# Kernel tuning notes

Hardware: AMD Instinct MI355X
Metric: run time of the kernel (lower is better)

The kernel has to match this reference:

```python
import jax, jax.numpy as jnp
import numpy as np

D_MODEL = 1024
NUM_HEADS = 16
DILATION = 2
SEG = 2048


def setup_inputs() -> dict:
    key = jax.random.key(0)
    k1, k2, k3, k4, k5 = jax.random.split(key, 5)
    B, S, D = 2, 8192, D_MODEL
    scale = 1.0 / np.sqrt(D)
    x = jax.random.normal(k1, (B, S, D), dtype=jnp.float32)
    wqkv = jax.random.normal(k2, (D, 3 * D), dtype=jnp.float32) * scale
    bqkv = jnp.zeros((3 * D,), dtype=jnp.float32)
    wo = jax.random.normal(k3, (D, D), dtype=jnp.float32) * scale
    bo = jnp.zeros((D,), dtype=jnp.float32)
    return {"x": x, "wqkv": wqkv, "bqkv": bqkv, "wo": wo, "bo": bo}


def reference(x, wqkv, bqkv, wo, bo):
    B, S, D = x.shape
    H = NUM_HEADS
    hd = D // H
    # segment reshape + dilated strided slice: [B, N, L, D]
    xs = x.reshape(B, -1, SEG, D)[:, :, ::DILATION, :]
    Bn, N, L, _ = xs.shape
    # fused QKV projection
    qkv = xs @ wqkv + bqkv                       # [B, N, L, 3D]
    q, k, v = jnp.split(qkv, 3, axis=-1)
    q = q.reshape(B, N, L, H, hd)
    k = k.reshape(B, N, L, H, hd)
    v = v.reshape(B, N, L, H, hd)
    scale = 1.0 / jnp.sqrt(jnp.asarray(hd, dtype=x.dtype))
    scores = jnp.einsum("bnqhd,bnkhd->bnhqk", q, k) * scale
    attn = jax.nn.softmax(scores, axis=-1)
    out = jnp.einsum("bnhqk,bnkhd->bnqhd", attn, v).reshape(B, N, L, D)
    out = out @ wo + bo                          # out projection
    return out.reshape(B, N * L, D)
```

## Files before the change

kernel.cpp:

```cpp
#include <hip/hip_runtime.h>
#include <hip/hip_bf16.h>
#include <stdint.h>

typedef __attribute__((ext_vector_type(8))) short short8;
typedef __attribute__((ext_vector_type(4))) float float4v;
typedef __attribute__((ext_vector_type(4))) unsigned int uint4v;
typedef unsigned short u16;

#if __has_builtin(__builtin_amdgcn_exp2f)
#define EXP2F(x) __builtin_amdgcn_exp2f(x)
#else
#define EXP2F(x) __expf(0.69314718056f * (x))
#endif

__device__ __forceinline__ u16 f2b(float f) {
    union { __hip_bfloat16 b; u16 u; } cv;
    cv.b = __float2bfloat16(f);
    return cv.u;
}

#define GLD16(g, l) __builtin_amdgcn_global_load_lds( \
    (const __attribute__((address_space(1))) void*)(g), \
    (__attribute__((address_space(3))) void*)(l), 16, 0, 0)

__global__ void convert_x(const float* __restrict__ x, u16* __restrict__ xb) {
    int id = blockIdx.x * 256 + threadIdx.x;
    int row = id >> 8;
    int c4 = id & 255;
    const float4* src = reinterpret_cast<const float4*>(x + (size_t)(2 * row) * 1024) + c4;
    float4 v = *src;
    ushort4 o;
    o.x = f2b(v.x); o.y = f2b(v.y); o.z = f2b(v.z); o.w = f2b(v.w);
    *(reinterpret_cast<ushort4*>(xb + (size_t)row * 1024) + c4) = o;
}

__global__ void transpose_convert(const float* __restrict__ in, u16* __restrict__ out,
                                  int K, int N) {
    __shared__ float tile[32][33];
    int n0 = blockIdx.x * 32, k0 = blockIdx.y * 32;
    int tx = threadIdx.x, ty = threadIdx.y;
#pragma unroll
    for (int i = 0; i < 4; i++)
        tile[ty + i * 8][tx] = in[(size_t)(k0 + ty + i * 8) * N + n0 + tx];
    __syncthreads();
#pragma unroll
    for (int i = 0; i < 4; i++)
        out[(size_t)(n0 + ty + i * 8) * K + k0 + tx] = f2b(tile[tx][ty + i * 8]);
}

template <int MODE>
__global__ __launch_bounds__(256) void gemm_bt(
    const u16* __restrict__ A, const u16* __restrict__ BT,
    const float* __restrict__ bias,
    float* __restrict__ Cf, u16* __restrict__ Cqk, u16* __restrict__ Cvt,
    int M, int N, int K) {
    __shared__ u16 As[128 * 32];
    __shared__ u16 Bs[128 * 32];
    const int tid = threadIdx.x;
    const int w = tid >> 6, l = tid & 63;
    const int q = l >> 4, c = l & 15;
    const int m0 = blockIdx.y * 128, n0 = blockIdx.x * 128;
    const int wm = (w >> 1) * 64, wn = (w & 1) * 64;

    const int srow = w * 16 + (l >> 2);
    const int scol = (l & 3) * 8;
    const u16* gA = A + (size_t)(m0 + srow) * K + scol;
    const u16* gB = BT + (size_t)(n0 + srow) * K + scol;

    float4v acc[4][4];
#pragma unroll
    for (int i = 0; i < 4; i++)
#pragma unroll
        for (int j = 0; j < 4; j++) acc[i][j] = {0.f, 0.f, 0.f, 0.f};

    char* AsB = (char*)&As[0];
    char* BsB = (char*)&Bs[0];

    for (int k0 = 0; k0 < K; k0 += 32) {
        __syncthreads();
        GLD16(gA + k0,                  AsB + w * 1024);
        GLD16(gA + (size_t)64 * K + k0, AsB + 4096 + w * 1024);
        GLD16(gB + k0,                  BsB + w * 1024);
        GLD16(gB + (size_t)64 * K + k0, BsB + 4096 + w * 1024);
        __syncthreads();
        short8 af[4], bf[4];
#pragma unroll
        for (int mt = 0; mt < 4; mt++)
            af[mt] = *reinterpret_cast<const short8*>(&As[(wm + mt * 16 + c) * 32 + q * 8]);
#pragma unroll
        for (int nt = 0; nt < 4; nt++)
            bf[nt] = *reinterpret_cast<const short8*>(&Bs[(wn + nt * 16 + c) * 32 + q * 8]);
#pragma unroll
        for (int mt = 0; mt < 4; mt++)
#pragma unroll
            for (int nt = 0; nt < 4; nt++)
                acc[mt][nt] = __builtin_amdgcn_mfma_f32_16x16x32_bf16(af[mt], bf[nt], acc[mt][nt], 0, 0, 0);
    }

    const int q4 = q * 4;
    if (MODE == 0) {
#pragma unroll
        for (int nt = 0; nt < 4; nt++) {
            int col = n0 + wn + nt * 16 + c;
            float bv = bias[col];
#pragma unroll
            for (int mt = 0; mt < 4; mt++) {
                int row = m0 + wm + mt * 16 + q4;
#pragma unroll
                for (int r = 0; r < 4; r++)
                    Cf[(size_t)(row + r) * N + col] = acc[mt][nt][r] + bv;
            }
        }
    } else {
        bool isV = (n0 + wn) >= 2048;
        float qscale = ((n0 + wn) < 1024) ? (0.125f * 1.44269504f) : 1.0f;
#pragma unroll
        for (int nt = 0; nt < 4; nt++) {
            int col = n0 + wn + nt * 16 + c;
            float bv = bias[col];
            if (!isV) {
#pragma unroll
                for (int mt = 0; mt < 4; mt++) {
                    int row = m0 + wm + mt * 16 + q4;
#pragma unroll
                    for (int r = 0; r < 4; r++)
                        Cqk[(size_t)(row + r) * 2048 + col] = f2b((acc[mt][nt][r] + bv) * qscale);
                }
            } else {
                int hd_ = col - 2048;
#pragma unroll
                for (int mt = 0; mt < 4; mt++) {
                    int row = m0 + wm + mt * 16 + q4;
                    int bn = row >> 10, key = row & 1023;
                    ushort4 pk;
                    pk.x = f2b(acc[mt][nt][0] + bv);
                    pk.y = f2b(acc[mt][nt][1] + bv);
                    pk.z = f2b(acc[mt][nt][2] + bv);
                    pk.w = f2b(acc[mt][nt][3] + bv);
                    *reinterpret_cast<ushort4*>(
                        &Cvt[((size_t)(bn << 10) + hd_) * 1024 + key]) = pk;
                }
            }
        }
    }
}

__global__ __launch_bounds__(256) void attn(const u16* __restrict__ qk,
                                            const u16* __restrict__ vt,
                                            u16* __restrict__ ob) {
    __shared__ u16 Ks[64 * 72];
    __shared__ u16 Vs[80 * 72];
    __shared__ u16 Ps[128 * 72];
    const int tid = threadIdx.x;
    const int w = tid >> 6, l = tid & 63, q = l >> 4, c = l & 15;
    const int qtile = blockIdx.x, combo = blockIdx.y;
    const int bn = combo >> 4, h = combo & 15;
    const int t0 = bn << 10;
    const int qoff = h << 6;
    const int koff = 1024 + (h << 6);
    const int vrow0 = combo << 6;
    const int qrow_base = t0 + qtile * 128 + w * 32;

    for (int idx = tid; idx < 16 * 72; idx += 256) {
        int rr = idx / 72, cc = idx - rr * 72;
        Vs[(64 + rr) * 72 + cc] = (rr == 0) ? (u16)0x3F80 : (u16)0;
    }

    short8 aq[2][2];
#pragma unroll
    for (int mt = 0; mt < 2; mt++)
#pragma unroll
        for (int ks = 0; ks < 2; ks++)
            aq[mt][ks] = *reinterpret_cast<const short8*>(
                qk + (size_t)(qrow_base + mt * 16 + c) * 2048 + qoff + ks * 32 + q * 8);

    float4v o_acc[2][4];
    float4v osum[2];
#pragma unroll
    for (int mt = 0; mt < 2; mt++) {
#pragma unroll
        for (int nt = 0; nt < 4; nt++) o_acc[mt][nt] = {0.f, 0.f, 0.f, 0.f};
        osum[mt] = {0.f, 0.f, 0.f, 0.f};
    }

    const int sr = tid >> 3;
    const int sc = (tid & 7) * 8;

    for (int chunk = 0; chunk < 16; chunk++) {
        const int key0 = chunk * 64;
        __syncthreads();
#pragma unroll
        for (int i = 0; i < 2; i++) {
            int r = sr + i * 32;
            uint4v kv = *reinterpret_cast<const uint4v*>(
                qk + (size_t)(t0 + key0 + r) * 2048 + koff + sc);
            *reinterpret_cast<uint4v*>(&Ks[r * 72 + sc]) = kv;
            uint4v vv = *reinterpret_cast<const uint4v*>(
                vt + (size_t)(vrow0 + r) * 1024 + key0 + sc);
            *reinterpret_cast<uint4v*>(&Vs[r * 72 + sc]) = vv;
        }
        __syncthreads();

        float4v s[2][4];
#pragma unroll
        for (int mt = 0; mt < 2; mt++)
#pragma unroll
            for (int nt = 0; nt < 4; nt++) s[mt][nt] = {0.f, 0.f, 0.f, 0.f};
#pragma unroll
        for (int ks = 0; ks < 2; ks++) {
            short8 bk[4];
#pragma unroll
            for (int nt = 0; nt < 4; nt++)
                bk[nt] = *reinterpret_cast<const short8*>(&Ks[(nt * 16 + c) * 72 + ks * 32 + q * 8]);
#pragma unroll
            for (int mt = 0; mt < 2; mt++)
#pragma unroll
                for (int nt = 0; nt < 4; nt++)
                    s[mt][nt] = __builtin_amdgcn_mfma_f32_16x16x32_bf16(aq[mt][ks], bk[nt], s[mt][nt], 0, 0, 0);
        }

#pragma unroll
        for (int mt = 0; mt < 2; mt++)
#pragma unroll
            for (int r = 0; r < 4; r++)
#pragma unroll
                for (int nt = 0; nt < 4; nt++)
                    Ps[(w * 32 + mt * 16 + q * 4 + r) * 72 + nt * 16 + c] =
                        f2b(EXP2F(s[mt][nt][r]));

#pragma unroll
        for (int ks = 0; ks < 2; ks++) {
            short8 pf[2], vf[4], v1;
#pragma unroll
            for (int mt = 0; mt < 2; mt++)
                pf[mt] = *reinterpret_cast<const short8*>(&Ps[(w * 32 + mt * 16 + c) * 72 + ks * 32 + q * 8]);
#pragma unroll
            for (int nt = 0; nt < 4; nt++)
                vf[nt] = *reinterpret_cast<const short8*>(&Vs[(nt * 16 + c) * 72 + ks * 32 + q * 8]);
            v1 = *reinterpret_cast<const short8*>(&Vs[(64 + c) * 72 + ks * 32 + q * 8]);
#pragma unroll
            for (int mt = 0; mt < 2; mt++) {
#pragma unroll
                for (int nt = 0; nt < 4; nt++)
                    o_acc[mt][nt] = __builtin_amdgcn_mfma_f32_16x16x32_bf16(pf[mt], vf[nt], o_acc[mt][nt], 0, 0, 0);
                osum[mt] = __builtin_amdgcn_mfma_f32_16x16x32_bf16(pf[mt], v1, osum[mt], 0, 0, 0);
            }
        }
    }

#pragma unroll
    for (int mt = 0; mt < 2; mt++) {
        float inv[4];
#pragma unroll
        for (int r = 0; r < 4; r++) {
            float lv = __shfl(osum[mt][r], tid & 48);
            inv[r] = 1.0f / lv;
        }
#pragma unroll
        for (int nt = 0; nt < 4; nt++)
#pragma unroll
            for (int r = 0; r < 4; r++) {
                int row = qrow_base + mt * 16 + q * 4 + r;
                int col = (h << 6) + nt * 16 + c;
                ob[(size_t)row * 1024 + col] = f2b(o_acc[mt][nt][r] * inv[r]);
            }
    }
}

extern "C" void kernel_launch(void* const* d_in, const int* in_sizes, int n_in,
                              void* d_out, int out_size, void* d_ws, size_t ws_size,
                              hipStream_t stream) {
    const float* x    = (const float*)d_in[0];
    const float* wqkv = (const float*)d_in[1];
    const float* bqkv = (const float*)d_in[2];
    const float* wo   = (const float*)d_in[3];
    const float* bo   = (const float*)d_in[4];
    float* out = (float*)d_out;
    char* ws = (char*)d_ws;

    u16* xb    = (u16*)(ws);
    u16* wqkvT = (u16*)(ws + 16777216);
    u16* woT   = (u16*)(ws + 23068672);
    u16* qkb   = (u16*)(ws + 25165824);
    u16* vtb   = (u16*)(ws + 58720256);
    u16* obuf  = (u16*)(ws + 75497472);

    convert_x<<<8192, 256, 0, stream>>>(x, xb);
    transpose_convert<<<dim3(96, 32), dim3(32, 8), 0, stream>>>(wqkv, wqkvT, 1024, 3072);
    transpose_convert<<<dim3(32, 32), dim3(32, 8), 0, stream>>>(wo, woT, 1024, 1024);
    gemm_bt<1><<<dim3(24, 64), 256, 0, stream>>>(xb, wqkvT, bqkv,
                                                 nullptr, qkb, vtb, 8192, 3072, 1024);
    attn<<<dim3(8, 128), 256, 0, stream>>>(qkb, vtb, obuf);
    gemm_bt<0><<<dim3(8, 64), 256, 0, stream>>>(obuf, woT, bo,
                                                out, nullptr, nullptr, 8192, 1024, 1024);
}
```

Baseline: 306.4 us.

## Load K/V MFMA fragments directly from global, dropping LDS staging and barriers

The attention kernel no longer stages each 64-key K and V chunk in shared memory. Each wave now loads its MFMA B-operand fragments straight from global memory into registers, which removes both per-chunk __syncthreads and the shared-memory round trip. The row-sum 'ones' operand is now built in registers rather than read from a padded LDS row. The cost is that all four waves fetch the same K/V data separately, so L1/L2 traffic rises and the reads are less coalesced. Global load latency is also now exposed directly in the inner loop.

```diff
diff --git a/kernel.cpp b/kernel.cpp
--- a/kernel.cpp
+++ b/kernel.cpp
@@ -148,8 +148,6 @@
 __global__ __launch_bounds__(256) void attn(const u16* __restrict__ qk,
                                             const u16* __restrict__ vt,
                                             u16* __restrict__ ob) {
-    __shared__ u16 Ks[64 * 72];
-    __shared__ u16 Vs[80 * 72];
     __shared__ u16 Ps[128 * 72];
     const int tid = threadIdx.x;
     const int w = tid >> 6, l = tid & 63, q = l >> 4, c = l & 15;
@@ -161,9 +159,11 @@
     const int vrow0 = combo << 6;
     const int qrow_base = t0 + qtile * 128 + w * 32;
 
-    for (int idx = tid; idx < 16 * 72; idx += 256) {
-        int rr = idx / 72, cc = idx - rr * 72;
-        Vs[(64 + rr) * 72 + cc] = (rr == 0) ? (u16)0x3F80 : (u16)0;
+    short8 v1;
+    {
+        u16 one = (c == 0) ? (u16)0x3F80 : (u16)0;
+#pragma unroll
+        for (int j = 0; j < 8; j++) v1[j] = (short)one;
     }
 
     short8 aq[2][2];
@@ -183,23 +183,19 @@
         osum[mt] = {0.f, 0.f, 0.f, 0.f};
     }
 
-    const int sr = tid >> 3;
-    const int sc = (tid & 7) * 8;
+    const u16* kfrag = qk + (size_t)(t0 + c) * 2048 + koff + q * 8;
+    const u16* vfrag = vt + (size_t)(vrow0 + c) * 1024 + q * 8;
 
     for (int chunk = 0; chunk < 16; chunk++) {
         const int key0 = chunk * 64;
-        __syncthreads();
-#pragma unroll
-        for (int i = 0; i < 2; i++) {
-            int r = sr + i * 32;
-            uint4v kv = *reinterpret_cast<const uint4v*>(
-                qk + (size_t)(t0 + key0 + r) * 2048 + koff + sc);
-            *reinterpret_cast<uint4v*>(&Ks[r * 72 + sc]) = kv;
-            uint4v vv = *reinterpret_cast<const uint4v*>(
-                vt + (size_t)(vrow0 + r) * 1024 + key0 + sc);
-            *reinterpret_cast<uint4v*>(&Vs[r * 72 + sc]) = vv;
-        }
-        __syncthreads();
+
+        short8 bk[2][4];
+#pragma unroll
+        for (int ks = 0; ks < 2; ks++)
+#pragma unroll
+            for (int nt = 0; nt < 4; nt++)
+                bk[ks][nt] = *reinterpret_cast<const short8*>(
+                    kfrag + (size_t)(key0 + nt * 16) * 2048 + ks * 32);
 
         float4v s[2][4];
 #pragma unroll
@@ -207,17 +203,20 @@
 #pragma unroll
             for (int nt = 0; nt < 4; nt++) s[mt][nt] = {0.f, 0.f, 0.f, 0.f};
 #pragma unroll
-        for (int ks = 0; ks < 2; ks++) {
-            short8 bk[4];
+        for (int ks = 0; ks < 2; ks++)
+#pragma unroll
+            for (int mt = 0; mt < 2; mt++)
+#pragma unroll
+                for (int nt = 0; nt < 4; nt++)
+                    s[mt][nt] = __builtin_amdgcn_mfma_f32_16x16x32_bf16(aq[mt][ks], bk[ks][nt], s[mt][nt], 0, 0, 0);
+
+        short8 vf[2][4];
+#pragma unroll
+        for (int ks = 0; ks < 2; ks++)
 #pragma unroll
             for (int nt = 0; nt < 4; nt++)
-                bk[nt] = *reinterpret_cast<const short8*>(&Ks[(nt * 16 + c) * 72 + ks * 32 + q * 8]);
-#pragma unroll
-            for (int mt = 0; mt < 2; mt++)
-#pragma unroll
-                for (int nt = 0; nt < 4; nt++)
-                    s[mt][nt] = __builtin_amdgcn_mfma_f32_16x16x32_bf16(aq[mt][ks], bk[nt], s[mt][nt], 0, 0, 0);
-        }
+                vf[ks][nt] = *reinterpret_cast<const short8*>(
+                    vfrag + (size_t)(nt * 16) * 1024 + key0 + ks * 32);
 
 #pragma unroll
         for (int mt = 0; mt < 2; mt++)
@@ -230,19 +229,16 @@
 
 #pragma unroll
         for (int ks = 0; ks < 2; ks++) {
-            short8 pf[2], vf[4], v1;
+            short8 pf[2];
 #pragma unroll
             for (int mt = 0; mt < 2; mt++)
-                pf[mt] = *reinterpret_cast<const short8*>(&Ps[(w * 32 + mt * 16 + c) * 72 + ks * 32 + q * 8]);
-#pragma unroll
-            for (int nt = 0; nt < 4; nt++)
-                vf[nt] = *reinterpret_cast<const short8*>(&Vs[(nt * 16 + c) * 72 + ks * 32 + q * 8]);
-            v1 = *reinterpret_cast<const short8*>(&Vs[(64 + c) * 72 + ks * 32 + q * 8]);
+                pf[mt] = *reinterpret_cast<const short8*>(
+                    &Ps[(w * 32 + mt * 16 + c) * 72 + ks * 32 + q * 8]);
 #pragma unroll
             for (int mt = 0; mt < 2; mt++) {
 #pragma unroll
                 for (int nt = 0; nt < 4; nt++)
-                    o_acc[mt][nt] = __builtin_amdgcn_mfma_f32_16x16x32_bf16(pf[mt], vf[nt], o_acc[mt][nt], 0, 0, 0);
+                    o_acc[mt][nt] = __builtin_amdgcn_mfma_f32_16x16x32_bf16(pf[mt], vf[ks][nt], o_acc[mt][nt], 0, 0, 0);
                 osum[mt] = __builtin_amdgcn_mfma_f32_16x16x32_bf16(pf[mt], v1, osum[mt], 0, 0, 0);
             }
         }
```

Measured after the change: 366.0 us. +19.5%, slower.

## Prefetch next K/V chunk into registers and build ones-vector in registers

Applied to the files above, without the earlier changes.

The attention kernel now issues the global loads for the next 64-key K/V chunk into registers before computing the current chunk. It writes them to shared memory after the PV MFMAs, so global latency overlaps with compute. The constant ones-vector used for the row-sum MFMA is built directly in registers instead of being stored in and read from an extra LDS region. This raises register pressure and keeps two barriers per iteration.

```diff
diff --git a/kernel.cpp b/kernel.cpp
--- a/kernel.cpp
+++ b/kernel.cpp
@@ -149,7 +149,7 @@
                                             const u16* __restrict__ vt,
                                             u16* __restrict__ ob) {
     __shared__ u16 Ks[64 * 72];
-    __shared__ u16 Vs[80 * 72];
+    __shared__ u16 Vs[64 * 72];
     __shared__ u16 Ps[128 * 72];
     const int tid = threadIdx.x;
     const int w = tid >> 6, l = tid & 63, q = l >> 4, c = l & 15;
@@ -161,9 +161,11 @@
     const int vrow0 = combo << 6;
     const int qrow_base = t0 + qtile * 128 + w * 32;
 
-    for (int idx = tid; idx < 16 * 72; idx += 256) {
-        int rr = idx / 72, cc = idx - rr * 72;
-        Vs[(64 + rr) * 72 + cc] = (rr == 0) ? (u16)0x3F80 : (u16)0;
+    short8 v1;
+    {
+        u16 one = (c == 0) ? (u16)0x3F80 : (u16)0;
+#pragma unroll
+        for (int j = 0; j < 8; j++) v1[j] = (short)one;
     }
 
     short8 aq[2][2];
@@ -186,20 +188,35 @@
     const int sr = tid >> 3;
     const int sc = (tid & 7) * 8;
 
+    uint4v kreg[2], vreg[2];
+#pragma unroll
+    for (int i = 0; i < 2; i++) {
+        int r = sr + i * 32;
+        kreg[i] = *reinterpret_cast<const uint4v*>(
+            qk + (size_t)(t0 + r) * 2048 + koff + sc);
+        vreg[i] = *reinterpret_cast<const uint4v*>(
+            vt + (size_t)(vrow0 + r) * 1024 + sc);
+    }
+#pragma unroll
+    for (int i = 0; i < 2; i++) {
+        int r = sr + i * 32;
+        *reinterpret_cast<uint4v*>(&Ks[r * 72 + sc]) = kreg[i];
+        *reinterpret_cast<uint4v*>(&Vs[r * 72 + sc]) = vreg[i];
+    }
+    __syncthreads();
+
     for (int chunk = 0; chunk < 16; chunk++) {
-        const int key0 = chunk * 64;
-        __syncthreads();
-#pragma unroll
-        for (int i = 0; i < 2; i++) {
-            int r = sr + i * 32;
-            uint4v kv = *reinterpret_cast<const uint4v*>(
-                qk + (size_t)(t0 + key0 + r) * 2048 + koff + sc);
-            *reinterpret_cast<uint4v*>(&Ks[r * 72 + sc]) = kv;
-            uint4v vv = *reinterpret_cast<const uint4v*>(
-                vt + (size_t)(vrow0 + r) * 1024 + key0 + sc);
-            *reinterpret_cast<uint4v*>(&Vs[r * 72 + sc]) = vv;
-        }
-        __syncthreads();
+        if (chunk < 15) {
+            const int key0n = (chunk + 1) * 64;
+#pragma unroll
+            for (int i = 0; i < 2; i++) {
+                int r = sr + i * 32;
+                kreg[i] = *reinterpret_cast<const uint4v*>(
+                    qk + (size_t)(t0 + key0n + r) * 2048 + koff + sc);
+                vreg[i] = *reinterpret_cast<const uint4v*>(
+                    vt + (size_t)(vrow0 + r) * 1024 + key0n + sc);
+            }
+        }
 
         float4v s[2][4];
 #pragma unroll
@@ -230,14 +247,14 @@
 
 #pragma unroll
         for (int ks = 0; ks < 2; ks++) {
-            short8 pf[2], vf[4], v1;
+            short8 pf[2], vf[4];
 #pragma unroll
             for (int mt = 0; mt < 2; mt++)
-                pf[mt] = *reinterpret_cast<const short8*>(&Ps[(w * 32 + mt * 16 + c) * 72 + ks * 32 + q * 8]);
+                pf[mt] = *reinterpret_cast<const short8*>(
+                    &Ps[(w * 32 + mt * 16 + c) * 72 + ks * 32 + q * 8]);
 #pragma unroll
             for (int nt = 0; nt < 4; nt++)
                 vf[nt] = *reinterpret_cast<const short8*>(&Vs[(nt * 16 + c) * 72 + ks * 32 + q * 8]);
-            v1 = *reinterpret_cast<const short8*>(&Vs[(64 + c) * 72 + ks * 32 + q * 8]);
 #pragma unroll
             for (int mt = 0; mt < 2; mt++) {
 #pragma unroll
@@ -245,6 +262,17 @@
                     o_acc[mt][nt] = __builtin_amdgcn_mfma_f32_16x16x32_bf16(pf[mt], vf[nt], o_acc[mt][nt], 0, 0, 0);
                 osum[mt] = __builtin_amdgcn_mfma_f32_16x16x32_bf16(pf[mt], v1, osum[mt], 0, 0, 0);
             }
+        }
+
+        if (chunk < 15) {
+            __syncthreads();
+#pragma unroll
+            for (int i = 0; i < 2; i++) {
+                int r = sr + i * 32;
+                *reinterpret_cast<uint4v*>(&Ks[r * 72 + sc]) = kreg[i];
+                *reinterpret_cast<uint4v*>(&Vs[r * 72 + sc]) = vreg[i];
+            }
+            __syncthreads();
         }
     }
 
```

New measurement: 278.9 us. 1.1x faster.
